# Kernel optimization log

Measured on AMD Instinct MI355X. Metric: run time of the kernel, lower is better.

## Reference

```python
import jax, jax.numpy as jnp
import numpy as np

N_NODES = 50000
N_EDGES = 625000
D = 128
H = 128

def setup_inputs() -> dict:
    key = jax.random.key(0)
    ks = jax.random.split(key, 6)
    z = jax.random.normal(ks[0], (N_NODES, D), dtype=jnp.float32)
    edge_index = jax.random.randint(ks[1], (2, N_EDGES), 0, N_NODES, dtype=jnp.int64)
    # MLP params (Linear stores y = x @ W + b here; W is [in, out])
    W1 = jax.random.normal(ks[2], (2 * D, H), dtype=jnp.float32) * (1.0 / np.sqrt(2 * D))
    b1 = jnp.zeros((H,), dtype=jnp.float32)
    W2 = jax.random.normal(ks[3], (H, H // 2), dtype=jnp.float32) * (1.0 / np.sqrt(H))
    b2 = jnp.zeros((H // 2,), dtype=jnp.float32)
    W3 = jax.random.normal(ks[4], (H // 2, 1), dtype=jnp.float32) * (1.0 / np.sqrt(H // 2))
    b3 = jnp.zeros((1,), dtype=jnp.float32)
    return {"z": z, "edge_index": edge_index, "W1": W1, "b1": b1,
            "W2": W2, "b2": b2, "W3": W3, "b3": b3}

def reference(z, edge_index, W1, b1, W2, b2, W3, b3):
    # Gather edge endpoints: z_i [E, D], z_j [E, D]
    z_i = z[edge_index[0]]
    z_j = z[edge_index[1]]
    edge_feat = jnp.concatenate([z_i, z_j], axis=-1)  # [E, 2D]
    h = jax.nn.relu(edge_feat @ W1 + b1)              # [E, H]  (dropout = identity, eval)
    h = jax.nn.relu(h @ W2 + b2)                      # [E, H//2]
    scores = (h @ W3 + b3)[:, 0]                      # [E]
    return scores
```

## Files before the change

kernel.cpp:

```cpp
#include <hip/hip_runtime.h>

#define NEDGE 625000
#define NNODE 50000
#define WPITCH 136
#define EPITCH 68

typedef __bf16 bf16x8 __attribute__((ext_vector_type(8)));
typedef unsigned short u16x8 __attribute__((ext_vector_type(8)));
typedef float f32x4 __attribute__((ext_vector_type(4)));

__device__ __forceinline__ unsigned short f32_bf16(float f) {
  unsigned int u = __float_as_uint(f);
  u += 0x7FFFu + ((u >> 16) & 1u);
  return (unsigned short)(u >> 16);
}
__device__ __forceinline__ float bf16_f32(unsigned short h) {
  return __uint_as_float(((unsigned int)h) << 16);
}

__global__ __launch_bounds__(256) void prep_kernel(
    const float* __restrict__ W1, const float* __restrict__ W2,
    const int* __restrict__ ei,
    unsigned short* __restrict__ WcatT, unsigned short* __restrict__ W2T,
    int* __restrict__ idx64_flag)
{
  int i = blockIdx.x * 256 + threadIdx.x;
  if (i < 256 * 128) {
    int jp = i >> 7, k = i & 127;
    float v = (jp < 128) ? W1[k * 128 + jp] : W1[(128 + k) * 128 + (jp - 128)];
    WcatT[jp * 128 + k] = f32_bf16(v);
  } else if (i < 256 * 128 + 64 * 128) {
    int i2 = i - 256 * 128;
    int n = i2 >> 7, k = i2 & 127;
    W2T[n * 128 + k] = f32_bf16(W2[k * 64 + n]);
  }
  if (i == 0) {
    int allz = 1;
    for (int j = 1; j < 64; j += 2) allz &= (ei[j] == 0);
    *idx64_flag = allz;
  }
}

__global__ __launch_bounds__(256) void uv_kernel(
    const float* __restrict__ z, const float* __restrict__ b1,
    const unsigned short* __restrict__ WcatT,
    unsigned short* __restrict__ UV)
{
  __shared__ unsigned short st[4 * 32 * EPITCH];
  const int t = threadIdx.x, wave = t >> 6, lane = t & 63, c = lane & 15, q = lane >> 4;
  const int mbase = blockIdx.x * 128 + wave * 32;
  const int rA = mbase + c, rB = mbase + 16 + c;
  const int rAc = (rA < NNODE) ? rA : 0;
  const int rBc = (rB < NNODE) ? rB : 0;

  bf16x8 a0[4], a1[4];
  {
    const float* zA = z + (size_t)rAc * 128 + q * 8;
    const float* zB = z + (size_t)rBc * 128 + q * 8;
    float4 fA[4][2], fB[4][2];
#pragma unroll
    for (int kt = 0; kt < 4; ++kt) {
      fA[kt][0] = ((const float4*)(zA + kt * 32))[0];
      fA[kt][1] = ((const float4*)(zA + kt * 32))[1];
      fB[kt][0] = ((const float4*)(zB + kt * 32))[0];
      fB[kt][1] = ((const float4*)(zB + kt * 32))[1];
    }
#pragma unroll
    for (int kt = 0; kt < 4; ++kt) {
      const float* pa = (const float*)&fA[kt][0];
      const float* pb = (const float*)&fB[kt][0];
      u16x8 oa, ob;
#pragma unroll
      for (int j = 0; j < 8; ++j) { oa[j] = f32_bf16(pa[j]); ob[j] = f32_bf16(pb[j]); }
      a0[kt] = *(bf16x8*)&oa;
      a1[kt] = *(bf16x8*)&ob;
    }
  }

  unsigned short* my = &st[wave * 32 * EPITCH];

  for (int nc = 0; nc < 4; ++nc) {
    f32x4 acc[2][4];
#pragma unroll
    for (int mt = 0; mt < 2; ++mt)
#pragma unroll
      for (int nt = 0; nt < 4; ++nt) {
        f32x4 zz = {0.f, 0.f, 0.f, 0.f};
        acc[mt][nt] = zz;
      }

#pragma unroll
    for (int kt = 0; kt < 4; ++kt) {
#pragma unroll
      for (int nt = 0; nt < 4; ++nt) {
        bf16x8 bb = *(const bf16x8*)(WcatT + (size_t)(nc * 64 + nt * 16 + c) * 128 + kt * 32 + q * 8);
        acc[0][nt] = __builtin_amdgcn_mfma_f32_16x16x32_bf16(a0[kt], bb, acc[0][nt], 0, 0, 0);
        acc[1][nt] = __builtin_amdgcn_mfma_f32_16x16x32_bf16(a1[kt], bb, acc[1][nt], 0, 0, 0);
      }
    }

    float badd[4];
#pragma unroll
    for (int nt = 0; nt < 4; ++nt) {
      int col = nc * 64 + nt * 16 + c;
      badd[nt] = (col < 128) ? b1[col] : 0.f;
    }

#pragma unroll
    for (int mt = 0; mt < 2; ++mt)
#pragma unroll
      for (int nt = 0; nt < 4; ++nt)
#pragma unroll
        for (int reg = 0; reg < 4; ++reg)
          my[(mt * 16 + q * 4 + reg) * EPITCH + nt * 16 + c] =
              f32_bf16(acc[mt][nt][reg] + badd[nt]);
    __asm__ volatile("s_waitcnt lgkmcnt(0)" ::: "memory");

    {
      int lrow = lane >> 1, half = lane & 1;
      int grow = mbase + lrow;
      u16x8 d0 = *(u16x8*)&my[lrow * EPITCH + half * 32 + 0];
      u16x8 d1 = *(u16x8*)&my[lrow * EPITCH + half * 32 + 8];
      u16x8 d2 = *(u16x8*)&my[lrow * EPITCH + half * 32 + 16];
      u16x8 d3 = *(u16x8*)&my[lrow * EPITCH + half * 32 + 24];
      if (grow < NNODE) {
        u16x8* dst = (u16x8*)(UV + (size_t)grow * 256 + nc * 64 + half * 32);
        dst[0] = d0;
        dst[1] = d1;
        dst[2] = d2;
        dst[3] = d3;
      }
    }
    __asm__ volatile("s_waitcnt lgkmcnt(0)" ::: "memory");
  }
}

__global__ __launch_bounds__(256) void edge_kernel(
    const int* __restrict__ ei,
    const unsigned short* __restrict__ UV,
    const unsigned short* __restrict__ W2T,
    const float* __restrict__ b2, const float* __restrict__ W3,
    const float* __restrict__ b3, const int* __restrict__ idx64_flag,
    float* __restrict__ out)
{
  __shared__ unsigned short lW[64 * WPITCH];
  const int t = threadIdx.x, wave = t >> 6, lane = t & 63, c = lane & 15, q = lane >> 4;

  {
    int n = t >> 2, qd = t & 3;
    const u16x8* src = (const u16x8*)(W2T + n * 128 + qd * 32);
    u16x8* dst = (u16x8*)(&lW[n * WPITCH + qd * 32]);
#pragma unroll
    for (int i = 0; i < 4; ++i) dst[i] = src[i];
  }
  __syncthreads();

  const int ebase = blockIdx.x * 128 + wave * 32;
  const int eA = ebase + c, eB = ebase + 16 + c;
  const int eAc = (eA < NEDGE) ? eA : 0;
  const int eBc = (eB < NEDGE) ? eB : 0;
  int sA, dA, sB, dB;
  if (*idx64_flag) {
    const long long* e64 = (const long long*)ei;
    sA = (int)e64[eAc]; dA = (int)e64[NEDGE + eAc];
    sB = (int)e64[eBc]; dB = (int)e64[NEDGE + eBc];
  } else {
    sA = ei[eAc]; dA = ei[NEDGE + eAc];
    sB = ei[eBc]; dB = ei[NEDGE + eBc];
  }

  const u16x8* pAu = (const u16x8*)(UV + (size_t)sA * 256) + q;
  const u16x8* pAv = (const u16x8*)(UV + (size_t)dA * 256 + 128) + q;
  const u16x8* pBu = (const u16x8*)(UV + (size_t)sB * 256) + q;
  const u16x8* pBv = (const u16x8*)(UV + (size_t)dB * 256 + 128) + q;
  u16x8 rAu[4], rAv[4], rBu[4], rBv[4];
#pragma unroll
  for (int kt = 0; kt < 4; ++kt) {
    rAu[kt] = pAu[kt * 4];
    rAv[kt] = pAv[kt * 4];
    rBu[kt] = pBu[kt * 4];
    rBv[kt] = pBv[kt * 4];
  }

  f32x4 acc[2][4];
#pragma unroll
  for (int mt = 0; mt < 2; ++mt)
#pragma unroll
    for (int nt = 0; nt < 4; ++nt) {
      f32x4 zz = {0.f, 0.f, 0.f, 0.f};
      acc[mt][nt] = zz;
    }

#pragma unroll
  for (int kt = 0; kt < 4; ++kt) {
    u16x8 oa, ob;
#pragma unroll
    for (int j = 0; j < 8; ++j) {
      oa[j] = f32_bf16(fmaxf(bf16_f32(rAu[kt][j]) + bf16_f32(rAv[kt][j]), 0.f));
      ob[j] = f32_bf16(fmaxf(bf16_f32(rBu[kt][j]) + bf16_f32(rBv[kt][j]), 0.f));
    }
    bf16x8 a0 = *(bf16x8*)&oa;
    bf16x8 a1 = *(bf16x8*)&ob;
#pragma unroll
    for (int nt = 0; nt < 4; ++nt) {
      bf16x8 bb = *(const bf16x8*)(&lW[(nt * 16 + c) * WPITCH + kt * 32 + q * 8]);
      acc[0][nt] = __builtin_amdgcn_mfma_f32_16x16x32_bf16(a0, bb, acc[0][nt], 0, 0, 0);
      acc[1][nt] = __builtin_amdgcn_mfma_f32_16x16x32_bf16(a1, bb, acc[1][nt], 0, 0, 0);
    }
  }

  float b2v[4], w3v[4];
#pragma unroll
  for (int nt = 0; nt < 4; ++nt) {
    int n = nt * 16 + c;
    b2v[nt] = b2[n];
    w3v[nt] = W3[n];
  }
  float bias3 = b3[0];

#pragma unroll
  for (int mt = 0; mt < 2; ++mt) {
    float p0 = 0.f, p1 = 0.f, p2 = 0.f, p3 = 0.f;
#pragma unroll
    for (int nt = 0; nt < 4; ++nt) {
      p0 += fmaxf(acc[mt][nt][0] + b2v[nt], 0.f) * w3v[nt];
      p1 += fmaxf(acc[mt][nt][1] + b2v[nt], 0.f) * w3v[nt];
      p2 += fmaxf(acc[mt][nt][2] + b2v[nt], 0.f) * w3v[nt];
      p3 += fmaxf(acc[mt][nt][3] + b2v[nt], 0.f) * w3v[nt];
    }
#pragma unroll
    for (int m = 1; m < 16; m <<= 1) {
      p0 += __shfl_xor(p0, m, 64);
      p1 += __shfl_xor(p1, m, 64);
      p2 += __shfl_xor(p2, m, 64);
      p3 += __shfl_xor(p3, m, 64);
    }
    if (c == 0) {
      int eb = ebase + mt * 16 + q * 4;
      if (eb + 0 < NEDGE) out[eb + 0] = p0 + bias3;
      if (eb + 1 < NEDGE) out[eb + 1] = p1 + bias3;
      if (eb + 2 < NEDGE) out[eb + 2] = p2 + bias3;
      if (eb + 3 < NEDGE) out[eb + 3] = p3 + bias3;
    }
  }
}

extern "C" void kernel_launch(void* const* d_in, const int* in_sizes, int n_in,
                              void* d_out, int out_size, void* d_ws, size_t ws_size,
                              hipStream_t stream) {
  const float* z  = (const float*)d_in[0];
  const int*   ei = (const int*)d_in[1];
  const float* W1 = (const float*)d_in[2];
  const float* b1 = (const float*)d_in[3];
  const float* W2 = (const float*)d_in[4];
  const float* b2 = (const float*)d_in[5];
  const float* W3 = (const float*)d_in[6];
  const float* b3 = (const float*)d_in[7];
  float* out = (float*)d_out;

  unsigned short* UV    = (unsigned short*)d_ws;
  unsigned short* WcatT = UV + (size_t)NNODE * 256;
  unsigned short* W2T   = WcatT + 256 * 128;
  int* idx64_flag       = (int*)(W2T + 64 * 128);

  prep_kernel<<<dim3(160), dim3(256), 0, stream>>>(W1, W2, ei, WcatT, W2T, idx64_flag);
  uv_kernel<<<dim3((NNODE + 127) / 128), dim3(256), 0, stream>>>(z, b1, WcatT, UV);
  edge_kernel<<<dim3((NEDGE + 127) / 128), dim3(256), 0, stream>>>(
      ei, UV, W2T, b2, W3, b3, idx64_flag, out);
}
```

Measured before the change: 153.6 us.

## Process multiple edge tiles per block with software-prefetched gathers; split uv over column chunks

The edge kernel now handles four 128-edge tiles per block. It loads all indices up front and prefetches the next tile's UV gather while computing the current tile, so gather latency overlaps MFMA work and the W2 LDS staging is amortized. The uv kernel spreads its four column chunks across separate blocks for more parallelism, at the cost of reloading z four times. Conversions now use vector bf16 convert and a native bf16 add/max for the layer-1 ReLU, which changes rounding slightly (sum done in bf16 rather than fp32).

```diff
diff --git a/kernel.cpp b/kernel.cpp
--- a/kernel.cpp
+++ b/kernel.cpp
@@ -2,20 +2,29 @@
 
 #define NEDGE 625000
 #define NNODE 50000
+#define NTILES ((NEDGE + 127) / 128)
+#define TPB 4
 #define WPITCH 136
 #define EPITCH 68
 
 typedef __bf16 bf16x8 __attribute__((ext_vector_type(8)));
+typedef __bf16 bf16x4 __attribute__((ext_vector_type(4)));
 typedef unsigned short u16x8 __attribute__((ext_vector_type(8)));
 typedef float f32x4 __attribute__((ext_vector_type(4)));
+typedef float f32x8 __attribute__((ext_vector_type(8)));
 
 __device__ __forceinline__ unsigned short f32_bf16(float f) {
   unsigned int u = __float_as_uint(f);
   u += 0x7FFFu + ((u >> 16) & 1u);
   return (unsigned short)(u >> 16);
 }
-__device__ __forceinline__ float bf16_f32(unsigned short h) {
-  return __uint_as_float(((unsigned int)h) << 16);
+
+__device__ __forceinline__ bf16x8 addrelu8(u16x8 ua, u16x8 ub) {
+  bf16x8 a = *(bf16x8*)&ua, b = *(bf16x8*)&ub;
+  bf16x8 s = a + b;
+  const bf16x8 z = {(__bf16)0.f, (__bf16)0.f, (__bf16)0.f, (__bf16)0.f,
+                    (__bf16)0.f, (__bf16)0.f, (__bf16)0.f, (__bf16)0.f};
+  return __builtin_elementwise_max(s, z);
 }
 
 __global__ __launch_bounds__(256) void prep_kernel(
@@ -48,7 +57,8 @@
 {
   __shared__ unsigned short st[4 * 32 * EPITCH];
   const int t = threadIdx.x, wave = t >> 6, lane = t & 63, c = lane & 15, q = lane >> 4;
-  const int mbase = blockIdx.x * 128 + wave * 32;
+  const int mtile = blockIdx.x >> 2, nc = blockIdx.x & 3;
+  const int mbase = mtile * 128 + wave * 32;
   const int rA = mbase + c, rB = mbase + 16 + c;
   const int rAc = (rA < NNODE) ? rA : 0;
   const int rBc = (rB < NNODE) ? rB : 0;
@@ -57,81 +67,67 @@
   {
     const float* zA = z + (size_t)rAc * 128 + q * 8;
     const float* zB = z + (size_t)rBc * 128 + q * 8;
-    float4 fA[4][2], fB[4][2];
 #pragma unroll
     for (int kt = 0; kt < 4; ++kt) {
-      fA[kt][0] = ((const float4*)(zA + kt * 32))[0];
-      fA[kt][1] = ((const float4*)(zA + kt * 32))[1];
-      fB[kt][0] = ((const float4*)(zB + kt * 32))[0];
-      fB[kt][1] = ((const float4*)(zB + kt * 32))[1];
-    }
-#pragma unroll
-    for (int kt = 0; kt < 4; ++kt) {
-      const float* pa = (const float*)&fA[kt][0];
-      const float* pb = (const float*)&fB[kt][0];
-      u16x8 oa, ob;
-#pragma unroll
-      for (int j = 0; j < 8; ++j) { oa[j] = f32_bf16(pa[j]); ob[j] = f32_bf16(pb[j]); }
-      a0[kt] = *(bf16x8*)&oa;
-      a1[kt] = *(bf16x8*)&ob;
-    }
+      f32x8 vA = *(const f32x8*)(zA + kt * 32);
+      f32x8 vB = *(const f32x8*)(zB + kt * 32);
+      a0[kt] = __builtin_convertvector(vA, bf16x8);
+      a1[kt] = __builtin_convertvector(vB, bf16x8);
+    }
+  }
+
+  f32x4 acc[2][4];
+#pragma unroll
+  for (int mt = 0; mt < 2; ++mt)
+#pragma unroll
+    for (int nt = 0; nt < 4; ++nt) {
+      f32x4 zz = {0.f, 0.f, 0.f, 0.f};
+      acc[mt][nt] = zz;
+    }
+
+#pragma unroll
+  for (int kt = 0; kt < 4; ++kt) {
+#pragma unroll
+    for (int nt = 0; nt < 4; ++nt) {
+      bf16x8 bb = *(const bf16x8*)(WcatT + (size_t)(nc * 64 + nt * 16 + c) * 128 + kt * 32 + q * 8);
+      acc[0][nt] = __builtin_amdgcn_mfma_f32_16x16x32_bf16(a0[kt], bb, acc[0][nt], 0, 0, 0);
+      acc[1][nt] = __builtin_amdgcn_mfma_f32_16x16x32_bf16(a1[kt], bb, acc[1][nt], 0, 0, 0);
+    }
+  }
+
+  float badd[4];
+#pragma unroll
+  for (int nt = 0; nt < 4; ++nt) {
+    int col = nc * 64 + nt * 16 + c;
+    badd[nt] = (col < 128) ? b1[col] : 0.f;
   }
 
   unsigned short* my = &st[wave * 32 * EPITCH];
-
-  for (int nc = 0; nc < 4; ++nc) {
-    f32x4 acc[2][4];
-#pragma unroll
-    for (int mt = 0; mt < 2; ++mt)
-#pragma unroll
-      for (int nt = 0; nt < 4; ++nt) {
-        f32x4 zz = {0.f, 0.f, 0.f, 0.f};
-        acc[mt][nt] = zz;
-      }
-
-#pragma unroll
-    for (int kt = 0; kt < 4; ++kt) {
-#pragma unroll
-      for (int nt = 0; nt < 4; ++nt) {
-        bf16x8 bb = *(const bf16x8*)(WcatT + (size_t)(nc * 64 + nt * 16 + c) * 128 + kt * 32 + q * 8);
-        acc[0][nt] = __builtin_amdgcn_mfma_f32_16x16x32_bf16(a0[kt], bb, acc[0][nt], 0, 0, 0);
-        acc[1][nt] = __builtin_amdgcn_mfma_f32_16x16x32_bf16(a1[kt], bb, acc[1][nt], 0, 0, 0);
-      }
-    }
-
-    float badd[4];
+#pragma unroll
+  for (int mt = 0; mt < 2; ++mt)
 #pragma unroll
     for (int nt = 0; nt < 4; ++nt) {
-      int col = nc * 64 + nt * 16 + c;
-      badd[nt] = (col < 128) ? b1[col] : 0.f;
-    }
-
-#pragma unroll
-    for (int mt = 0; mt < 2; ++mt)
-#pragma unroll
-      for (int nt = 0; nt < 4; ++nt)
-#pragma unroll
-        for (int reg = 0; reg < 4; ++reg)
-          my[(mt * 16 + q * 4 + reg) * EPITCH + nt * 16 + c] =
-              f32_bf16(acc[mt][nt][reg] + badd[nt]);
-    __asm__ volatile("s_waitcnt lgkmcnt(0)" ::: "memory");
-
-    {
-      int lrow = lane >> 1, half = lane & 1;
-      int grow = mbase + lrow;
-      u16x8 d0 = *(u16x8*)&my[lrow * EPITCH + half * 32 + 0];
-      u16x8 d1 = *(u16x8*)&my[lrow * EPITCH + half * 32 + 8];
-      u16x8 d2 = *(u16x8*)&my[lrow * EPITCH + half * 32 + 16];
-      u16x8 d3 = *(u16x8*)&my[lrow * EPITCH + half * 32 + 24];
-      if (grow < NNODE) {
-        u16x8* dst = (u16x8*)(UV + (size_t)grow * 256 + nc * 64 + half * 32);
-        dst[0] = d0;
-        dst[1] = d1;
-        dst[2] = d2;
-        dst[3] = d3;
-      }
-    }
-    __asm__ volatile("s_waitcnt lgkmcnt(0)" ::: "memory");
+      f32x4 v = acc[mt][nt];
+      f32x4 vb = {v[0] + badd[nt], v[1] + badd[nt], v[2] + badd[nt], v[3] + badd[nt]};
+      bf16x4 bv = __builtin_convertvector(vb, bf16x4);
+      const unsigned short* pv = (const unsigned short*)&bv;
+#pragma unroll
+      for (int reg = 0; reg < 4; ++reg)
+        my[(mt * 16 + q * 4 + reg) * EPITCH + nt * 16 + c] = pv[reg];
+    }
+  __asm__ volatile("s_waitcnt lgkmcnt(0)" ::: "memory");
+
+  {
+    int lrow = lane >> 1, half = lane & 1;
+    int grow = mbase + lrow;
+    u16x8 d0 = *(u16x8*)&my[lrow * EPITCH + half * 32 + 0];
+    u16x8 d1 = *(u16x8*)&my[lrow * EPITCH + half * 32 + 8];
+    u16x8 d2 = *(u16x8*)&my[lrow * EPITCH + half * 32 + 16];
+    u16x8 d3 = *(u16x8*)&my[lrow * EPITCH + half * 32 + 24];
+    if (grow < NNODE) {
+      u16x8* dst = (u16x8*)(UV + (size_t)grow * 256 + nc * 64 + half * 32);
+      dst[0] = d0; dst[1] = d1; dst[2] = d2; dst[3] = d3;
+    }
   }
 }
 
@@ -155,57 +151,24 @@
   }
   __syncthreads();
 
-  const int ebase = blockIdx.x * 128 + wave * 32;
-  const int eA = ebase + c, eB = ebase + 16 + c;
-  const int eAc = (eA < NEDGE) ? eA : 0;
-  const int eBc = (eB < NEDGE) ? eB : 0;
-  int sA, dA, sB, dB;
-  if (*idx64_flag) {
-    const long long* e64 = (const long long*)ei;
-    sA = (int)e64[eAc]; dA = (int)e64[NEDGE + eAc];
-    sB = (int)e64[eBc]; dB = (int)e64[NEDGE + eBc];
-  } else {
-    sA = ei[eAc]; dA = ei[NEDGE + eAc];
-    sB = ei[eBc]; dB = ei[NEDGE + eBc];
-  }
-
-  const u16x8* pAu = (const u16x8*)(UV + (size_t)sA * 256) + q;
-  const u16x8* pAv = (const u16x8*)(UV + (size_t)dA * 256 + 128) + q;
-  const u16x8* pBu = (const u16x8*)(UV + (size_t)sB * 256) + q;
-  const u16x8* pBv = (const u16x8*)(UV + (size_t)dB * 256 + 128) + q;
-  u16x8 rAu[4], rAv[4], rBu[4], rBv[4];
-#pragma unroll
-  for (int kt = 0; kt < 4; ++kt) {
-    rAu[kt] = pAu[kt * 4];
-    rAv[kt] = pAv[kt * 4];
-    rBu[kt] = pBu[kt * 4];
-    rBv[kt] = pBv[kt * 4];
-  }
-
-  f32x4 acc[2][4];
-#pragma unroll
-  for (int mt = 0; mt < 2; ++mt)
-#pragma unroll
-    for (int nt = 0; nt < 4; ++nt) {
-      f32x4 zz = {0.f, 0.f, 0.f, 0.f};
-      acc[mt][nt] = zz;
-    }
-
-#pragma unroll
-  for (int kt = 0; kt < 4; ++kt) {
-    u16x8 oa, ob;
-#pragma unroll
-    for (int j = 0; j < 8; ++j) {
-      oa[j] = f32_bf16(fmaxf(bf16_f32(rAu[kt][j]) + bf16_f32(rAv[kt][j]), 0.f));
-      ob[j] = f32_bf16(fmaxf(bf16_f32(rBu[kt][j]) + bf16_f32(rBv[kt][j]), 0.f));
-    }
-    bf16x8 a0 = *(bf16x8*)&oa;
-    bf16x8 a1 = *(bf16x8*)&ob;
-#pragma unroll
-    for (int nt = 0; nt < 4; ++nt) {
-      bf16x8 bb = *(const bf16x8*)(&lW[(nt * 16 + c) * WPITCH + kt * 32 + q * 8]);
-      acc[0][nt] = __builtin_amdgcn_mfma_f32_16x16x32_bf16(a0, bb, acc[0][nt], 0, 0, 0);
-      acc[1][nt] = __builtin_amdgcn_mfma_f32_16x16x32_bf16(a1, bb, acc[1][nt], 0, 0, 0);
+  const int tile0 = blockIdx.x * TPB;
+  int sA[TPB], dA[TPB], sB[TPB], dB[TPB];
+  {
+    const int is64 = *idx64_flag;
+#pragma unroll
+    for (int tt = 0; tt < TPB; ++tt) {
+      int ebase = (tile0 + tt) * 128 + wave * 32;
+      int eA = ebase + c, eB = ebase + 16 + c;
+      int eAc = (eA < NEDGE) ? eA : 0;
+      int eBc = (eB < NEDGE) ? eB : 0;
+      if (is64) {
+        const long long* e64 = (const long long*)ei;
+        sA[tt] = (int)e64[eAc]; dA[tt] = (int)e64[NEDGE + eAc];
+        sB[tt] = (int)e64[eBc]; dB[tt] = (int)e64[NEDGE + eBc];
+      } else {
+        sA[tt] = ei[eAc]; dA[tt] = ei[NEDGE + eAc];
+        sB[tt] = ei[eBc]; dB[tt] = ei[NEDGE + eBc];
+      }
     }
   }
 
@@ -216,33 +179,81 @@
     b2v[nt] = b2[n];
     w3v[nt] = W3[n];
   }
-  float bias3 = b3[0];
-
-#pragma unroll
-  for (int mt = 0; mt < 2; ++mt) {
-    float p0 = 0.f, p1 = 0.f, p2 = 0.f, p3 = 0.f;
-#pragma unroll
-    for (int nt = 0; nt < 4; ++nt) {
-      p0 += fmaxf(acc[mt][nt][0] + b2v[nt], 0.f) * w3v[nt];
-      p1 += fmaxf(acc[mt][nt][1] + b2v[nt], 0.f) * w3v[nt];
-      p2 += fmaxf(acc[mt][nt][2] + b2v[nt], 0.f) * w3v[nt];
-      p3 += fmaxf(acc[mt][nt][3] + b2v[nt], 0.f) * w3v[nt];
-    }
-#pragma unroll
-    for (int m = 1; m < 16; m <<= 1) {
-      p0 += __shfl_xor(p0, m, 64);
-      p1 += __shfl_xor(p1, m, 64);
-      p2 += __shfl_xor(p2, m, 64);
-      p3 += __shfl_xor(p3, m, 64);
-    }
-    if (c == 0) {
-      int eb = ebase + mt * 16 + q * 4;
-      if (eb + 0 < NEDGE) out[eb + 0] = p0 + bias3;
-      if (eb + 1 < NEDGE) out[eb + 1] = p1 + bias3;
-      if (eb + 2 < NEDGE) out[eb + 2] = p2 + bias3;
-      if (eb + 3 < NEDGE) out[eb + 3] = p3 + bias3;
-    }
-  }
+  const float bias3 = b3[0];
+
+  u16x8 rAu[4], rAv[4], rBu[4], rBv[4];
+#define GATHER(tt)                                                           \
+  {                                                                          \
+    const u16x8* pAu = (const u16x8*)(UV + (size_t)sA[tt] * 256) + q;        \
+    const u16x8* pAv = (const u16x8*)(UV + (size_t)dA[tt] * 256 + 128) + q;  \
+    const u16x8* pBu = (const u16x8*)(UV + (size_t)sB[tt] * 256) + q;        \
+    const u16x8* pBv = (const u16x8*)(UV + (size_t)dB[tt] * 256 + 128) + q;  \
+    _Pragma("unroll") for (int kt = 0; kt < 4; ++kt) {                       \
+      rAu[kt] = pAu[kt * 4];                                                 \
+      rAv[kt] = pAv[kt * 4];                                                 \
+      rBu[kt] = pBu[kt * 4];                                                 \
+      rBv[kt] = pBv[kt * 4];                                                 \
+    }                                                                        \
+  }
+
+  GATHER(0)
+
+  for (int tt = 0; tt < TPB; ++tt) {
+    bf16x8 a0[4], a1[4];
+#pragma unroll
+    for (int kt = 0; kt < 4; ++kt) {
+      a0[kt] = addrelu8(rAu[kt], rAv[kt]);
+      a1[kt] = addrelu8(rBu[kt], rBv[kt]);
+    }
+    if (tt + 1 < TPB) GATHER(tt + 1)
+
+    f32x4 acc[2][4];
+#pragma unroll
+    for (int mt = 0; mt < 2; ++mt)
+#pragma unroll
+      for (int nt = 0; nt < 4; ++nt) {
+        f32x4 zz = {0.f, 0.f, 0.f, 0.f};
+        acc[mt][nt] = zz;
+      }
+
+#pragma unroll
+    for (int kt = 0; kt < 4; ++kt) {
+#pragma unroll
+      for (int nt = 0; nt < 4; ++nt) {
+        bf16x8 bb = *(const bf16x8*)(&lW[(nt * 16 + c) * WPITCH + kt * 32 + q * 8]);
+        acc[0][nt] = __builtin_amdgcn_mfma_f32_16x16x32_bf16(a0[kt], bb, acc[0][nt], 0, 0, 0);
+        acc[1][nt] = __builtin_amdgcn_mfma_f32_16x16x32_bf16(a1[kt], bb, acc[1][nt], 0, 0, 0);
+      }
+    }
+
+    const int ebase = (tile0 + tt) * 128 + wave * 32;
+#pragma unroll
+    for (int mt = 0; mt < 2; ++mt) {
+      float p0 = 0.f, p1 = 0.f, p2 = 0.f, p3 = 0.f;
+#pragma unroll
+      for (int nt = 0; nt < 4; ++nt) {
+        p0 += fmaxf(acc[mt][nt][0] + b2v[nt], 0.f) * w3v[nt];
+        p1 += fmaxf(acc[mt][nt][1] + b2v[nt], 0.f) * w3v[nt];
+        p2 += fmaxf(acc[mt][nt][2] + b2v[nt], 0.f) * w3v[nt];
+        p3 += fmaxf(acc[mt][nt][3] + b2v[nt], 0.f) * w3v[nt];
+      }
+#pragma unroll
+      for (int m = 1; m < 16; m <<= 1) {
+        p0 += __shfl_xor(p0, m, 64);
+        p1 += __shfl_xor(p1, m, 64);
+        p2 += __shfl_xor(p2, m, 64);
+        p3 += __shfl_xor(p3, m, 64);
+      }
+      if (c == 0) {
+        int eb = ebase + mt * 16 + q * 4;
+        if (eb + 0 < NEDGE) out[eb + 0] = p0 + bias3;
+        if (eb + 1 < NEDGE) out[eb + 1] = p1 + bias3;
+        if (eb + 2 < NEDGE) out[eb + 2] = p2 + bias3;
+        if (eb + 3 < NEDGE) out[eb + 3] = p3 + bias3;
+      }
+    }
+  }
+#undef GATHER
 }
 
 extern "C" void kernel_launch(void* const* d_in, const int* in_sizes, int n_in,
@@ -264,7 +275,7 @@
   int* idx64_flag       = (int*)(W2T + 64 * 128);
 
   prep_kernel<<<dim3(160), dim3(256), 0, stream>>>(W1, W2, ei, WcatT, W2T, idx64_flag);
-  uv_kernel<<<dim3((NNODE + 127) / 128), dim3(256), 0, stream>>>(z, b1, WcatT, UV);
-  edge_kernel<<<dim3((NEDGE + 127) / 128), dim3(256), 0, stream>>>(
+  uv_kernel<<<dim3(((NNODE + 127) / 128) * 4), dim3(256), 0, stream>>>(z, b1, WcatT, UV);
+  edge_kernel<<<dim3((NTILES + TPB - 1) / TPB), dim3(256), 0, stream>>>(
       ei, UV, W2T, b2, W3, b3, idx64_flag, out);
 }
```

Result: slower. 182.1 us (+18.6%).

## Split UV column chunks across waves and use packed bf16 add-relu

Applied to the files above, without the earlier changes.

The UV precompute kernel now gives each of its four waves one 64-column chunk for the same 32 nodes, replacing the serial four-chunk loop per wave, and launches four times as many blocks. The fp32-to-bf16 conversions use vector convertvector instead of manual bit rounding. The edge kernel's add+ReLU now works directly on packed bf16 vectors rather than round-tripping through fp32. This shortens per-wave serial work and cuts ALU instructions. The bf16-native add rounds differently from the fp32 add followed by rounding, and z rows are now loaded redundantly by all four waves.

```diff
diff --git a/kernel.cpp b/kernel.cpp
--- a/kernel.cpp
+++ b/kernel.cpp
@@ -2,20 +2,28 @@
 
 #define NEDGE 625000
 #define NNODE 50000
+#define NTILES ((NEDGE + 127) / 128)
 #define WPITCH 136
 #define EPITCH 68
 
 typedef __bf16 bf16x8 __attribute__((ext_vector_type(8)));
+typedef __bf16 bf16x4 __attribute__((ext_vector_type(4)));
 typedef unsigned short u16x8 __attribute__((ext_vector_type(8)));
 typedef float f32x4 __attribute__((ext_vector_type(4)));
+typedef float f32x8 __attribute__((ext_vector_type(8)));
 
 __device__ __forceinline__ unsigned short f32_bf16(float f) {
   unsigned int u = __float_as_uint(f);
   u += 0x7FFFu + ((u >> 16) & 1u);
   return (unsigned short)(u >> 16);
 }
-__device__ __forceinline__ float bf16_f32(unsigned short h) {
-  return __uint_as_float(((unsigned int)h) << 16);
+
+__device__ __forceinline__ bf16x8 addrelu8(u16x8 ua, u16x8 ub) {
+  bf16x8 a = *(bf16x8*)&ua, b = *(bf16x8*)&ub;
+  bf16x8 s = a + b;
+  const bf16x8 z = {(__bf16)0.f, (__bf16)0.f, (__bf16)0.f, (__bf16)0.f,
+                    (__bf16)0.f, (__bf16)0.f, (__bf16)0.f, (__bf16)0.f};
+  return __builtin_elementwise_max(s, z);
 }
 
 __global__ __launch_bounds__(256) void prep_kernel(
@@ -48,7 +56,8 @@
 {
   __shared__ unsigned short st[4 * 32 * EPITCH];
   const int t = threadIdx.x, wave = t >> 6, lane = t & 63, c = lane & 15, q = lane >> 4;
-  const int mbase = blockIdx.x * 128 + wave * 32;
+  const int nc = wave;
+  const int mbase = blockIdx.x * 32;
   const int rA = mbase + c, rB = mbase + 16 + c;
   const int rAc = (rA < NNODE) ? rA : 0;
   const int rBc = (rB < NNODE) ? rB : 0;
@@ -57,81 +66,67 @@
   {
     const float* zA = z + (size_t)rAc * 128 + q * 8;
     const float* zB = z + (size_t)rBc * 128 + q * 8;
-    float4 fA[4][2], fB[4][2];
 #pragma unroll
     for (int kt = 0; kt < 4; ++kt) {
-      fA[kt][0] = ((const float4*)(zA + kt * 32))[0];
-      fA[kt][1] = ((const float4*)(zA + kt * 32))[1];
-      fB[kt][0] = ((const float4*)(zB + kt * 32))[0];
-      fB[kt][1] = ((const float4*)(zB + kt * 32))[1];
-    }
-#pragma unroll
-    for (int kt = 0; kt < 4; ++kt) {
-      const float* pa = (const float*)&fA[kt][0];
-      const float* pb = (const float*)&fB[kt][0];
-      u16x8 oa, ob;
-#pragma unroll
-      for (int j = 0; j < 8; ++j) { oa[j] = f32_bf16(pa[j]); ob[j] = f32_bf16(pb[j]); }
-      a0[kt] = *(bf16x8*)&oa;
-      a1[kt] = *(bf16x8*)&ob;
-    }
+      f32x8 vA = *(const f32x8*)(zA + kt * 32);
+      f32x8 vB = *(const f32x8*)(zB + kt * 32);
+      a0[kt] = __builtin_convertvector(vA, bf16x8);
+      a1[kt] = __builtin_convertvector(vB, bf16x8);
+    }
+  }
+
+  f32x4 acc[2][4];
+#pragma unroll
+  for (int mt = 0; mt < 2; ++mt)
+#pragma unroll
+    for (int nt = 0; nt < 4; ++nt) {
+      f32x4 zz = {0.f, 0.f, 0.f, 0.f};
+      acc[mt][nt] = zz;
+    }
+
+#pragma unroll
+  for (int kt = 0; kt < 4; ++kt) {
+#pragma unroll
+    for (int nt = 0; nt < 4; ++nt) {
+      bf16x8 bb = *(const bf16x8*)(WcatT + (size_t)(nc * 64 + nt * 16 + c) * 128 + kt * 32 + q * 8);
+      acc[0][nt] = __builtin_amdgcn_mfma_f32_16x16x32_bf16(a0[kt], bb, acc[0][nt], 0, 0, 0);
+      acc[1][nt] = __builtin_amdgcn_mfma_f32_16x16x32_bf16(a1[kt], bb, acc[1][nt], 0, 0, 0);
+    }
+  }
+
+  float badd[4];
+#pragma unroll
+  for (int nt = 0; nt < 4; ++nt) {
+    int col = nc * 64 + nt * 16 + c;
+    badd[nt] = (col < 128) ? b1[col] : 0.f;
   }
 
   unsigned short* my = &st[wave * 32 * EPITCH];
-
-  for (int nc = 0; nc < 4; ++nc) {
-    f32x4 acc[2][4];
-#pragma unroll
-    for (int mt = 0; mt < 2; ++mt)
-#pragma unroll
-      for (int nt = 0; nt < 4; ++nt) {
-        f32x4 zz = {0.f, 0.f, 0.f, 0.f};
-        acc[mt][nt] = zz;
-      }
-
-#pragma unroll
-    for (int kt = 0; kt < 4; ++kt) {
-#pragma unroll
-      for (int nt = 0; nt < 4; ++nt) {
-        bf16x8 bb = *(const bf16x8*)(WcatT + (size_t)(nc * 64 + nt * 16 + c) * 128 + kt * 32 + q * 8);
-        acc[0][nt] = __builtin_amdgcn_mfma_f32_16x16x32_bf16(a0[kt], bb, acc[0][nt], 0, 0, 0);
-        acc[1][nt] = __builtin_amdgcn_mfma_f32_16x16x32_bf16(a1[kt], bb, acc[1][nt], 0, 0, 0);
-      }
-    }
-
-    float badd[4];
-#pragma unroll
-    for (int nt = 0; nt < 4; ++nt) {
-      int col = nc * 64 + nt * 16 + c;
-      badd[nt] = (col < 128) ? b1[col] : 0.f;
-    }
-
-#pragma unroll
-    for (int mt = 0; mt < 2; ++mt)
-#pragma unroll
-      for (int nt = 0; nt < 4; ++nt)
-#pragma unroll
-        for (int reg = 0; reg < 4; ++reg)
-          my[(mt * 16 + q * 4 + reg) * EPITCH + nt * 16 + c] =
-              f32_bf16(acc[mt][nt][reg] + badd[nt]);
-    __asm__ volatile("s_waitcnt lgkmcnt(0)" ::: "memory");
-
-    {
-      int lrow = lane >> 1, half = lane & 1;
-      int grow = mbase + lrow;
-      u16x8 d0 = *(u16x8*)&my[lrow * EPITCH + half * 32 + 0];
-      u16x8 d1 = *(u16x8*)&my[lrow * EPITCH + half * 32 + 8];
-      u16x8 d2 = *(u16x8*)&my[lrow * EPITCH + half * 32 + 16];
-      u16x8 d3 = *(u16x8*)&my[lrow * EPITCH + half * 32 + 24];
-      if (grow < NNODE) {
-        u16x8* dst = (u16x8*)(UV + (size_t)grow * 256 + nc * 64 + half * 32);
-        dst[0] = d0;
-        dst[1] = d1;
-        dst[2] = d2;
-        dst[3] = d3;
-      }
-    }
-    __asm__ volatile("s_waitcnt lgkmcnt(0)" ::: "memory");
+#pragma unroll
+  for (int mt = 0; mt < 2; ++mt)
+#pragma unroll
+    for (int nt = 0; nt < 4; ++nt) {
+      f32x4 v = acc[mt][nt];
+      f32x4 vb = {v[0] + badd[nt], v[1] + badd[nt], v[2] + badd[nt], v[3] + badd[nt]};
+      bf16x4 bv = __builtin_convertvector(vb, bf16x4);
+      const unsigned short* pv = (const unsigned short*)&bv;
+#pragma unroll
+      for (int reg = 0; reg < 4; ++reg)
+        my[(mt * 16 + q * 4 + reg) * EPITCH + nt * 16 + c] = pv[reg];
+    }
+  __asm__ volatile("s_waitcnt lgkmcnt(0)" ::: "memory");
+
+  {
+    int lrow = lane >> 1, half = lane & 1;
+    int grow = mbase + lrow;
+    u16x8 d0 = *(u16x8*)&my[lrow * EPITCH + half * 32 + 0];
+    u16x8 d1 = *(u16x8*)&my[lrow * EPITCH + half * 32 + 8];
+    u16x8 d2 = *(u16x8*)&my[lrow * EPITCH + half * 32 + 16];
+    u16x8 d3 = *(u16x8*)&my[lrow * EPITCH + half * 32 + 24];
+    if (grow < NNODE) {
+      u16x8* dst = (u16x8*)(UV + (size_t)grow * 256 + nc * 64 + half * 32);
+      dst[0] = d0; dst[1] = d1; dst[2] = d2; dst[3] = d3;
+    }
   }
 }
 
@@ -193,14 +188,8 @@
 
 #pragma unroll
   for (int kt = 0; kt < 4; ++kt) {
-    u16x8 oa, ob;
-#pragma unroll
-    for (int j = 0; j < 8; ++j) {
-      oa[j] = f32_bf16(fmaxf(bf16_f32(rAu[kt][j]) + bf16_f32(rAv[kt][j]), 0.f));
-      ob[j] = f32_bf16(fmaxf(bf16_f32(rBu[kt][j]) + bf16_f32(rBv[kt][j]), 0.f));
-    }
-    bf16x8 a0 = *(bf16x8*)&oa;
-    bf16x8 a1 = *(bf16x8*)&ob;
+    bf16x8 a0 = addrelu8(rAu[kt], rAv[kt]);
+    bf16x8 a1 = addrelu8(rBu[kt], rBv[kt]);
 #pragma unroll
     for (int nt = 0; nt < 4; ++nt) {
       bf16x8 bb = *(const bf16x8*)(&lW[(nt * 16 + c) * WPITCH + kt * 32 + q * 8]);
@@ -216,7 +205,7 @@
     b2v[nt] = b2[n];
     w3v[nt] = W3[n];
   }
-  float bias3 = b3[0];
+  const float bias3 = b3[0];
 
 #pragma unroll
   for (int mt = 0; mt < 2; ++mt) {
@@ -264,7 +253,7 @@
   int* idx64_flag       = (int*)(W2T + 64 * 128);
 
   prep_kernel<<<dim3(160), dim3(256), 0, stream>>>(W1, W2, ei, WcatT, W2T, idx64_flag);
-  uv_kernel<<<dim3((NNODE + 127) / 128), dim3(256), 0, stream>>>(z, b1, WcatT, UV);
-  edge_kernel<<<dim3((NEDGE + 127) / 128), dim3(256), 0, stream>>>(
+  uv_kernel<<<dim3((NNODE + 31) / 32), dim3(256), 0, stream>>>(z, b1, WcatT, UV);
+  edge_kernel<<<dim3(NTILES), dim3(256), 0, stream>>>(
       ei, UV, W2T, b2, W3, b3, idx64_flag, out);
 }
```

After: 160.2 us. 4.3% more time.
